# Kernel optimization log

Hardware: AMD Instinct MI355X
Metric: run time of the kernel (lower is better)

## Reference

```python
import jax, jax.numpy as jnp
import numpy as np
from jax import lax

STATE_SIZE = 80
HIDDEN = 512
NC = 1
H = W = 32
STEPS = 64  # steps_range=(64,64)
THRESH = 0.01


def _maxpool3(x):
    # MaxPool2d(3, stride=1, padding=1) on NCHW
    return lax.reduce_window(x, -jnp.inf, lax.max, (1, 1, 3, 3), (1, 1, 1, 1), 'SAME')


def _conv3x3(x, w, b):
    y = lax.conv_general_dilated(x, w, (1, 1), 'SAME',
                                 dimension_numbers=('NCHW', 'OIHW', 'NCHW'))
    return y + b[None, :, None, None]


def _conv1x1(x, w, b):
    # w: (O, I, 1, 1) -> pointwise einsum
    return jnp.einsum('oi,bihw->bohw', w[:, :, 0, 0], x) + b[None, :, None, None]


def setup_inputs() -> dict:
    key = jax.random.key(0)
    ks = jax.random.split(key, 7)
    z = jax.random.normal(ks[0], (8, 100, 1, 1), dtype=jnp.float32)
    W1 = jax.random.normal(ks[1], (HIDDEN, STATE_SIZE, 3, 3), jnp.float32) / np.sqrt(STATE_SIZE * 9)
    b1 = jax.random.normal(ks[2], (HIDDEN,), jnp.float32) * 0.01
    W2 = jax.random.normal(ks[3], (HIDDEN, HIDDEN, 1, 1), jnp.float32) / np.sqrt(HIDDEN)
    b2 = jax.random.normal(ks[4], (HIDDEN,), jnp.float32) * 0.01
    # original code zero-inits the last conv; use small random weights so grads flow
    W3 = jax.random.normal(ks[5], (STATE_SIZE, HIDDEN, 1, 1), jnp.float32) * (0.01 / np.sqrt(HIDDEN))
    b3 = jax.random.normal(ks[6], (STATE_SIZE,), jnp.float32) * 0.001
    return {'z': z, 'W1': W1, 'b1': b1, 'W2': W2, 'b2': b2, 'W3': W3, 'b3': b3}


def _forward(z, W1, b1, W2, b2, W3, b3):
    N = z.shape[0]
    cH, cW = H // 2, W // 2
    state = jnp.zeros((N, STATE_SIZE, H, W), dtype=z.dtype)
    init_hidden = z[:, :STATE_SIZE - 1, 0, 0]  # (N, 79)
    state = state.at[:, 1:, cH, cW].set(init_hidden)
    state = state.at[:, 0, cH, cW].set(1.0)

    keys = jax.random.split(jax.random.key(42), STEPS)

    def ca_step(state, step_key):
        pre_living = _maxpool3(state[:, 0:1]) > THRESH
        perception = _conv3x3(state, W1, b1)
        h = jax.nn.relu(_conv1x1(perception, W2, b2))
        updates = _conv1x1(h, W3, b3)
        # stochastic update with p=1 (rand < 1 is always True, kept for fidelity)
        mask = jax.random.uniform(step_key, (state.shape[0], 1, H, W)) < 1.0
        state = state + mask.astype(state.dtype) * updates
        post_living = _maxpool3(state[:, 0:1]) > THRESH
        living = (post_living & pre_living).astype(state.dtype)
        return state * living, None

    state, _ = lax.scan(ca_step, state, keys)
    return state[:, :NC]  # (N, 1, H, W)


def reference(z, W1, b1, W2, b2, W3, b3):
    return _forward(z, W1, b1, W2, b2, W3, b3)
```

## Files before the change

### kernel.cpp

```cpp
#include <hip/hip_runtime.h>


#define NPIX 8192
#define T_ALIVE 0.01f

typedef _Float16 f16;
typedef __attribute__((ext_vector_type(8)))  _Float16 h8_t;
typedef __attribute__((ext_vector_type(4)))  _Float16 h4_t;
typedef __attribute__((ext_vector_type(16))) float    fx16;

__global__ __launch_bounds__(256) void tr512(
    const float* __restrict__ W2, float* __restrict__ W2T)
{
    __shared__ float t[32][33];
    const int bx = blockIdx.x & 15, by = blockIdx.x >> 4;
    const int x = threadIdx.x & 31, y8 = threadIdx.x >> 5;
#pragma unroll
    for (int r = 0; r < 32; r += 8)
        t[r + y8][x] = W2[(size_t)(by * 32 + r + y8) * 512 + bx * 32 + x];
    __syncthreads();
#pragma unroll
    for (int r = 0; r < 32; r += 8)
        W2T[(size_t)(bx * 32 + r + y8) * 512 + by * 32 + x] = t[x][r + y8];
}

__global__ __launch_bounds__(256) void wc32(
    const float* __restrict__ W2T, const float* __restrict__ W1,
    float* __restrict__ Wc)
{
    __shared__ float As[16][32];
    __shared__ float Bs[16][32];
    const int tid = threadIdx.x;
    const int ty = tid >> 3, tx = tid & 7;
    const int m0 = blockIdx.y * 32, n0 = blockIdx.x * 32;
    float acc[4] = {0.f, 0.f, 0.f, 0.f};

    for (int k0 = 0; k0 < 512; k0 += 16) {
#pragma unroll
        for (int t = 0; t < 2; ++t) {
            const int idx = tid + t * 256;
            const int r = idx >> 5, c = idx & 31;
            As[r][c] = W2T[(size_t)(k0 + r) * 512 + m0 + c];
            const int n = n0 + c;
            Bs[r][c] = (n < 720) ? W1[(size_t)(k0 + r) * 720 + n] : 0.f;
        }
        __syncthreads();
#pragma unroll
        for (int kk = 0; kk < 16; ++kk) {
            const float a = As[kk][ty];
#pragma unroll
            for (int j = 0; j < 4; ++j)
                acc[j] = fmaf(a, Bs[kk][tx * 4 + j], acc[j]);
        }
        __syncthreads();
    }
    const int m = m0 + ty;
#pragma unroll
    for (int j = 0; j < 4; ++j) {
        const int n = n0 + tx * 4 + j;
        if (n < 720) Wc[(size_t)m * 720 + n] = acc[j];
    }
}

__global__ __launch_bounds__(256) void bc_k(
    const float* __restrict__ W2, const float* __restrict__ b1,
    const float* __restrict__ b2, float* __restrict__ bc)
{
    const int m = blockIdx.x * 256 + threadIdx.x;
    if (m >= 512) return;
    float a = b2[m];
    for (int h = 0; h < 512; ++h) a += W2[m * 512 + h] * b1[h];
    bc[m] = a;
}

__global__ __launch_bounds__(256) void swz_wc2(
    const float* __restrict__ Wc, f16* __restrict__ Wcsw2)
{
    const int idx = blockIdx.x * 256 + threadIdx.x;
    if (idx >= 45 * 16 * 64) return;
    const int lane = idx & 63;
    const int t = idx >> 6;
    const int mtg = t & 15, ks = t >> 4;
    const int m = mtg * 32 + (lane & 31);
    const int k0 = ks * 16 + (lane >> 5) * 8;
    h8_t v;
#pragma unroll
    for (int j = 0; j < 8; ++j) {
        const int kp = k0 + j;
        const int tap = kp / 80, ci = kp - tap * 80;
        v[j] = (f16)Wc[(size_t)m * 720 + ci * 9 + tap];
    }
    *(h8_t*)(Wcsw2 + (size_t)idx * 8) = v;
}

__global__ __launch_bounds__(256) void swz_w32(
    const float* __restrict__ W3, f16* __restrict__ W3sw2)
{
    const int idx = blockIdx.x * 256 + threadIdx.x;
    if (idx >= 32 * 3 * 64) return;
    const int lane = idx & 63;
    const int t = idx >> 6;
    const int mt = t % 3, ks2 = t / 3;
    const int m = mt * 32 + (lane & 31);
    const int k0 = ks2 * 16 + (lane >> 5) * 8;
    h8_t v;
#pragma unroll
    for (int j = 0; j < 8; ++j)
        v[j] = (f16)((m < 80) ? W3[(size_t)m * 512 + k0 + j] : 0.f);
    *(h8_t*)(W3sw2 + (size_t)idx * 8) = v;
}

__global__ __launch_bounds__(256) void seed_k(
    const float* __restrict__ z, float* __restrict__ Sf32,
    f16* __restrict__ Smf16)
{
    const int idx = blockIdx.x * 256 + threadIdx.x;
    if (idx >= 640) return;
    const int b = idx / 80, c = idx - b * 80;
    const int n = b * 1024 + 16 * 32 + 16;
    const float v = (c == 0) ? 1.f : z[b * 100 + (c - 1)];
    Sf32[(size_t)c * NPIX + n] = v;
    Smf16[(size_t)n * 80 + c] = (f16)v;
}

__global__ __launch_bounds__(512) void kA(
    const f16* __restrict__ Smf16, const f16* __restrict__ Wcsw2,
    const float* __restrict__ bc, const f16* __restrict__ W3sw2,
    const float* __restrict__ b3,
    const float* __restrict__ Sold, float* __restrict__ U)
{
    __shared__ f16   msT[8160];
    __shared__ f16   Hsw[16384];
    __shared__ float bcL[512];
    __shared__ float b3L[80];

    const int tid = threadIdx.x;
    const int lane = tid & 63, w = tid >> 6;
    const int li = lane & 31, q2 = lane >> 5;
    const int blk = blockIdx.x;
    const int b = blk >> 5, y = blk & 31;
    const int gb = b * 1024;

    if (tid < 512) bcL[tid] = bc[tid];
    if (tid < 80)  b3L[tid] = b3[tid];

    for (int idx = tid; idx < 1020; idx += 512) {
        const int p = idx / 10, cc = idx - p * 10;
        const int r = p / 34, xi = p - r * 34;
        const int gx = xi - 1, yy = y - 1 + r;
        h8_t v;
        if (((unsigned)yy < 32u) & ((unsigned)gx < 32u)) {
            v = *(const h8_t*)(Smf16 + (size_t)(gb + yy * 32 + gx) * 80 + cc * 8);
        } else {
#pragma unroll
            for (int j = 0; j < 8; ++j) v[j] = (f16)0.f;
        }
        *(h8_t*)(msT + (size_t)(cc * 102 + p) * 8) = v;
    }
    __syncthreads();

    int pxh[9];
#pragma unroll
    for (int t = 0; t < 9; ++t)
        pxh[t] = ((t / 3) * 34 + li + (t % 3)) * 8;

    fx16 acc[2];
#pragma unroll
    for (int i = 0; i < 2; ++i)
#pragma unroll
        for (int r = 0; r < 16; ++r) acc[i][r] = 0.f;

    h8_t abuf[8][2];
#pragma unroll
    for (int pk = 0; pk < 8; ++pk)
#pragma unroll
        for (int i = 0; i < 2; ++i)
            abuf[pk][i] = *(const h8_t*)(Wcsw2 +
                (((size_t)pk * 16 + (w * 2 + i)) * 64 + lane) * 8);

#pragma unroll
    for (int ks = 0; ks < 45; ++ks) {
        const int o0 = 2 * ks, o1 = 2 * ks + 1;
        const int a0 = (o0 % 10) * 816 + pxh[o0 / 10];
        const int a1 = (o1 % 10) * 816 + pxh[o1 / 10];
        const h8_t bf = *(const h8_t*)(msT + (q2 ? a1 : a0));
        h8_t av[2];
#pragma unroll
        for (int i = 0; i < 2; ++i) av[i] = abuf[ks & 7][i];
        if (ks + 8 < 45) {
#pragma unroll
            for (int i = 0; i < 2; ++i)
                abuf[ks & 7][i] = *(const h8_t*)(Wcsw2 +
                    (((size_t)(ks + 8) * 16 + (w * 2 + i)) * 64 + lane) * 8);
        }
#pragma unroll
        for (int i = 0; i < 2; ++i)
            acc[i] = __builtin_amdgcn_mfma_f32_32x32x16_f16(
                av[i], bf, acc[i], 0, 0, 0);
    }

#pragma unroll
    for (int i = 0; i < 2; ++i) {
#pragma unroll
        for (int aa = 0; aa < 4; ++aa) {
            const int chl = i * 32 + 8 * aa + 4 * q2;
            const int co = w * 8 + i * 4 + aa;
            h4_t v4;
#pragma unroll
            for (int rb = 0; rb < 4; ++rb)
                v4[rb] = (f16)fmaxf(acc[i][aa * 4 + rb] + bcL[w * 64 + chl + rb], 0.f);
            *(h4_t*)(Hsw + ((size_t)co * 32 + li) * 8 + 4 * q2) = v4;
        }
    }
    __syncthreads();

    if (w < 3) {
        const int mt = w;
        h8_t ar[8];
#pragma unroll
        for (int pk = 0; pk < 8; ++pk)
            ar[pk] = *(const h8_t*)(W3sw2 +
                (((size_t)pk * 3 + mt) * 64 + lane) * 8);

        fx16 acc3;
#pragma unroll
        for (int r = 0; r < 16; ++r) acc3[r] = 0.f;
#pragma unroll
        for (int ks2 = 0; ks2 < 32; ++ks2) {
            const h8_t bf = *(const h8_t*)(Hsw +
                ((size_t)(ks2 * 2 + q2) * 32 + li) * 8);
            const h8_t a = ar[ks2 & 7];
            if (ks2 + 8 < 32)
                ar[ks2 & 7] = *(const h8_t*)(W3sw2 +
                    (((size_t)(ks2 + 8) * 3 + mt) * 64 + lane) * 8);
            acc3 = __builtin_amdgcn_mfma_f32_32x32x16_f16(a, bf, acc3, 0, 0, 0);
        }

        const size_t px = (size_t)(gb + y * 32 + li);
#pragma unroll
        for (int aa = 0; aa < 4; ++aa)
#pragma unroll
            for (int rb = 0; rb < 4; ++rb) {
                const int ch = mt * 32 + rb + 8 * aa + 4 * q2;
                if (ch < 80) {
                    const size_t idx = (size_t)ch * NPIX + px;
                    U[idx] = Sold[idx] + acc3[aa * 4 + rb] + b3L[ch];
                }
            }
    }
}

__global__ __launch_bounds__(256) void kB(
    const float* __restrict__ U, const float* __restrict__ Sold,
    float* __restrict__ Snew, f16* __restrict__ Smf16,
    float* __restrict__ dout, int last)
{
    __shared__ float alphaO3[96];
    __shared__ float alphaN3[96];
    __shared__ float livef[32];

    const int tid = threadIdx.x;
    const int blk = blockIdx.x;
    const int b = blk >> 5, y = blk & 31;
    const int gb = b * 1024;
    const int base = gb + y * 32;

    if (tid < 96) {
        const int r = tid >> 5, x = tid & 31, yy = y - 1 + r;
        if ((unsigned)yy < 32u) {
            alphaO3[tid] = Sold[gb + yy * 32 + x];
            alphaN3[tid] = U[gb + yy * 32 + x];
        } else {
            alphaO3[tid] = -1e30f;
            alphaN3[tid] = -1e30f;
        }
    }
    __syncthreads();

    if (tid < 32) {
        float mN = -1e30f, mO = -1e30f;
#pragma unroll
        for (int r = 0; r < 3; ++r)
#pragma unroll
            for (int dx = -1; dx <= 1; ++dx) {
                const int xx = tid + dx;
                if ((unsigned)xx < 32u) {
                    mN = fmaxf(mN, alphaN3[r * 32 + xx]);
                    mO = fmaxf(mO, alphaO3[r * 32 + xx]);
                }
            }
        livef[tid] = (mN > T_ALIVE && mO > T_ALIVE) ? 1.f : 0.f;
    }
    __syncthreads();

    for (int q = tid; q < 640; q += 256) {
        const int cq = q >> 5, x = q & 31;
        const float lv = livef[x];
        const size_t pxg = (size_t)(base + x);
        h4_t v4;
        float v0 = 0.f;
#pragma unroll
        for (int rb = 0; rb < 4; ++rb) {
            const int ch = cq * 4 + rb;
            const size_t idx = (size_t)ch * NPIX + pxg;
            const float v = U[idx] * lv;
            Snew[idx] = v;
            v4[rb] = (f16)v;
            if (rb == 0) v0 = v;
        }
        *(h4_t*)(Smf16 + pxg * 80 + cq * 4) = v4;
        if (last && cq == 0) dout[pxg] = v0;
    }
}

extern "C" void kernel_launch(void* const* d_in, const int* in_sizes, int n_in,
                              void* d_out, int out_size, void* d_ws, size_t ws_size,
                              hipStream_t stream)
{
    const float* z  = (const float*)d_in[0];
    const float* W1 = (const float*)d_in[1];
    const float* b1 = (const float*)d_in[2];
    const float* W2 = (const float*)d_in[3];
    const float* b2 = (const float*)d_in[4];
    const float* W3 = (const float*)d_in[5];
    const float* b3 = (const float*)d_in[6];

    char* ws = (char*)d_ws;
    float* S0    = (float*)ws;  ws += (size_t)80 * NPIX * 4;
    float* S1    = (float*)ws;  ws += (size_t)80 * NPIX * 4;
    f16*   Sm0   = (f16*)ws;   ws += (size_t)NPIX * 80 * 2;
    f16*   Sm1   = (f16*)ws;   ws += (size_t)NPIX * 80 * 2;
    float* Ubuf  = (float*)ws;  ws += (size_t)80 * NPIX * 4;
    float* bc    = (float*)ws;  ws += 512 * 4;
    float* Wc    = (float*)ws;  ws += (size_t)512 * 720 * 4;
    float* W2T   = (float*)ws;  ws += (size_t)512 * 512 * 4;
    f16*   Wcsw2 = (f16*)ws;   ws += (size_t)45 * 16 * 64 * 8 * 2;
    f16*   W3sw2 = (f16*)ws;   ws += (size_t)32 * 3 * 64 * 8 * 2;

    hipMemsetAsync(S0, 0, (size_t)80 * NPIX * 4, stream);
    hipMemsetAsync(Sm0, 0, (size_t)NPIX * 80 * 2, stream);
    seed_k<<<3, 256, 0, stream>>>(z, S0, Sm0);
    tr512<<<256, 256, 0, stream>>>(W2, W2T);
    wc32<<<dim3(23, 16), 256, 0, stream>>>(W2T, W1, Wc);
    bc_k<<<2, 256, 0, stream>>>(W2, b1, b2, bc);
    swz_wc2<<<180, 256, 0, stream>>>(Wc, Wcsw2);
    swz_w32<<<24, 256, 0, stream>>>(W3, W3sw2);

    float* Scur = S0;  float* Snxt = S1;
    f16*   Mcur = Sm0; f16*   Mnxt = Sm1;
    for (int s = 0; s < 64; ++s) {
        kA<<<256, 512, 0, stream>>>(Mcur, Wcsw2, bc, W3sw2, b3, Scur, Ubuf);
        kB<<<256, 256, 0, stream>>>(Ubuf, Scur, Snxt, Mnxt,
                                    (float*)d_out, (s == 63) ? 1 : 0);
        float* t = Scur; Scur = Snxt; Snxt = t;
        f16*   m = Mcur; Mcur = Mnxt; Mnxt = m;
    }
}
```

Baseline: 1.143 ms.

## Fuse living-mask update into the compute kernel, dropping separate per-step mask kernel

Merges the per-step mask/writeback kernel into the main conv/MLP kernel. Each block now recomputes the living mask for its 3-row halo from the unmasked update buffer and the previous alive channel, and builds the f16 shared-memory tile directly from fp32 global data. A small final kernel applies the last mask. This halves the launches per step and removes the separate f16 state copy and its round trip, at the cost of redundant halo mask work and strided fp32 gathers into shared memory.

```diff
diff --git a/kernel.cpp b/kernel.cpp
--- a/kernel.cpp
+++ b/kernel.cpp
@@ -110,29 +110,33 @@
     *(h8_t*)(W3sw2 + (size_t)idx * 8) = v;
 }
 
-__global__ __launch_bounds__(256) void seed_k(
-    const float* __restrict__ z, float* __restrict__ Sf32,
-    f16* __restrict__ Smf16)
+__global__ __launch_bounds__(256) void seed2(
+    const float* __restrict__ z, float* __restrict__ U0,
+    float* __restrict__ A0)
 {
     const int idx = blockIdx.x * 256 + threadIdx.x;
     if (idx >= 640) return;
     const int b = idx / 80, c = idx - b * 80;
     const int n = b * 1024 + 16 * 32 + 16;
     const float v = (c == 0) ? 1.f : z[b * 100 + (c - 1)];
-    Sf32[(size_t)c * NPIX + n] = v;
-    Smf16[(size_t)n * 80 + c] = (f16)v;
-}
-
-__global__ __launch_bounds__(512) void kA(
-    const f16* __restrict__ Smf16, const f16* __restrict__ Wcsw2,
-    const float* __restrict__ bc, const f16* __restrict__ W3sw2,
-    const float* __restrict__ b3,
-    const float* __restrict__ Sold, float* __restrict__ U)
+    U0[(size_t)c * NPIX + n] = v;
+    if (c == 0) A0[n] = 1.f;
+}
+
+__global__ __launch_bounds__(512) void kS(
+    const f16* __restrict__ Wcsw2, const float* __restrict__ bc,
+    const f16* __restrict__ W3sw2, const float* __restrict__ b3,
+    const float* __restrict__ Uin, const float* __restrict__ Ain,
+    float* __restrict__ Uout, float* __restrict__ Aout)
 {
     __shared__ f16   msT[8160];
     __shared__ f16   Hsw[16384];
     __shared__ float bcL[512];
     __shared__ float b3L[80];
+    __shared__ float SrowL[2560];
+    __shared__ float N5[160];
+    __shared__ float A5[160];
+    __shared__ float live3[96];
 
     const int tid = threadIdx.x;
     const int lane = tid & 63, w = tid >> 6;
@@ -141,35 +145,6 @@
     const int b = blk >> 5, y = blk & 31;
     const int gb = b * 1024;
 
-    if (tid < 512) bcL[tid] = bc[tid];
-    if (tid < 80)  b3L[tid] = b3[tid];
-
-    for (int idx = tid; idx < 1020; idx += 512) {
-        const int p = idx / 10, cc = idx - p * 10;
-        const int r = p / 34, xi = p - r * 34;
-        const int gx = xi - 1, yy = y - 1 + r;
-        h8_t v;
-        if (((unsigned)yy < 32u) & ((unsigned)gx < 32u)) {
-            v = *(const h8_t*)(Smf16 + (size_t)(gb + yy * 32 + gx) * 80 + cc * 8);
-        } else {
-#pragma unroll
-            for (int j = 0; j < 8; ++j) v[j] = (f16)0.f;
-        }
-        *(h8_t*)(msT + (size_t)(cc * 102 + p) * 8) = v;
-    }
-    __syncthreads();
-
-    int pxh[9];
-#pragma unroll
-    for (int t = 0; t < 9; ++t)
-        pxh[t] = ((t / 3) * 34 + li + (t % 3)) * 8;
-
-    fx16 acc[2];
-#pragma unroll
-    for (int i = 0; i < 2; ++i)
-#pragma unroll
-        for (int r = 0; r < 16; ++r) acc[i][r] = 0.f;
-
     h8_t abuf[8][2];
 #pragma unroll
     for (int pk = 0; pk < 8; ++pk)
@@ -177,6 +152,70 @@
         for (int i = 0; i < 2; ++i)
             abuf[pk][i] = *(const h8_t*)(Wcsw2 +
                 (((size_t)pk * 16 + (w * 2 + i)) * 64 + lane) * 8);
+
+    bcL[tid] = bc[tid];
+    if (tid < 80) b3L[tid] = b3[tid];
+
+    if (tid < 160) {
+        const int r = tid >> 5, x = tid & 31, yy = y - 2 + r;
+        const bool ok = ((unsigned)yy < 32u);
+        N5[tid] = ok ? Uin[gb + yy * 32 + x] : -1e30f;
+        A5[tid] = ok ? Ain[gb + yy * 32 + x] : -1e30f;
+    }
+    {
+        h8_t zz;
+#pragma unroll
+        for (int j = 0; j < 8; ++j) zz[j] = (f16)0.f;
+        for (int i = tid; i < 1020; i += 512)
+            *(h8_t*)(msT + (size_t)i * 8) = zz;
+    }
+    __syncthreads();
+
+    if (tid < 96) {
+        const int r = tid >> 5, x = tid & 31;
+        float mN = -1e30f, mA = -1e30f;
+#pragma unroll
+        for (int rr = 0; rr < 3; ++rr)
+#pragma unroll
+            for (int dx = -1; dx <= 1; ++dx) {
+                const int xx = x + dx;
+                if ((unsigned)xx < 32u) {
+                    mN = fmaxf(mN, N5[(r + rr) * 32 + xx]);
+                    mA = fmaxf(mA, A5[(r + rr) * 32 + xx]);
+                }
+            }
+        live3[tid] = (mN > T_ALIVE && mA > T_ALIVE) ? 1.f : 0.f;
+    }
+    __syncthreads();
+
+#pragma unroll
+    for (int it = 0; it < 15; ++it) {
+        const int e = tid + it * 512;
+        const int x = e & 31;
+        const int t2 = e >> 5;
+        const int r = t2 / 80, ch = t2 - r * 80;
+        const int yy = y - 1 + r;
+        float v = 0.f;
+        if ((unsigned)yy < 32u)
+            v = Uin[(size_t)ch * NPIX + gb + yy * 32 + x] * live3[r * 32 + x];
+        msT[(size_t)((ch >> 3) * 102 + r * 34 + x + 1) * 8 + (ch & 7)] = (f16)v;
+        if (r == 1) {
+            SrowL[ch * 32 + x] = v;
+            if (ch == 0) Aout[gb + y * 32 + x] = v;
+        }
+    }
+    __syncthreads();
+
+    int pxh[9];
+#pragma unroll
+    for (int t = 0; t < 9; ++t)
+        pxh[t] = ((t / 3) * 34 + li + (t % 3)) * 8;
+
+    fx16 acc[2];
+#pragma unroll
+    for (int i = 0; i < 2; ++i)
+#pragma unroll
+        for (int r = 0; r < 16; ++r) acc[i][r] = 0.f;
 
 #pragma unroll
     for (int ks = 0; ks < 45; ++ks) {
@@ -243,73 +282,46 @@
             for (int rb = 0; rb < 4; ++rb) {
                 const int ch = mt * 32 + rb + 8 * aa + 4 * q2;
                 if (ch < 80) {
-                    const size_t idx = (size_t)ch * NPIX + px;
-                    U[idx] = Sold[idx] + acc3[aa * 4 + rb] + b3L[ch];
+                    Uout[(size_t)ch * NPIX + px] =
+                        SrowL[ch * 32 + li] + acc3[aa * 4 + rb] + b3L[ch];
                 }
             }
     }
 }
 
-__global__ __launch_bounds__(256) void kB(
-    const float* __restrict__ U, const float* __restrict__ Sold,
-    float* __restrict__ Snew, f16* __restrict__ Smf16,
-    float* __restrict__ dout, int last)
-{
-    __shared__ float alphaO3[96];
-    __shared__ float alphaN3[96];
-    __shared__ float livef[32];
-
+__global__ __launch_bounds__(128) void kF(
+    const float* __restrict__ Uf, const float* __restrict__ Af,
+    float* __restrict__ dout)
+{
+    __shared__ float N3[96];
+    __shared__ float A3[96];
     const int tid = threadIdx.x;
     const int blk = blockIdx.x;
     const int b = blk >> 5, y = blk & 31;
     const int gb = b * 1024;
-    const int base = gb + y * 32;
 
     if (tid < 96) {
         const int r = tid >> 5, x = tid & 31, yy = y - 1 + r;
-        if ((unsigned)yy < 32u) {
-            alphaO3[tid] = Sold[gb + yy * 32 + x];
-            alphaN3[tid] = U[gb + yy * 32 + x];
-        } else {
-            alphaO3[tid] = -1e30f;
-            alphaN3[tid] = -1e30f;
-        }
+        const bool ok = ((unsigned)yy < 32u);
+        N3[tid] = ok ? Uf[gb + yy * 32 + x] : -1e30f;
+        A3[tid] = ok ? Af[gb + yy * 32 + x] : -1e30f;
     }
     __syncthreads();
 
     if (tid < 32) {
-        float mN = -1e30f, mO = -1e30f;
-#pragma unroll
-        for (int r = 0; r < 3; ++r)
+        float mN = -1e30f, mA = -1e30f;
+#pragma unroll
+        for (int rr = 0; rr < 3; ++rr)
 #pragma unroll
             for (int dx = -1; dx <= 1; ++dx) {
                 const int xx = tid + dx;
                 if ((unsigned)xx < 32u) {
-                    mN = fmaxf(mN, alphaN3[r * 32 + xx]);
-                    mO = fmaxf(mO, alphaO3[r * 32 + xx]);
+                    mN = fmaxf(mN, N3[rr * 32 + xx]);
+                    mA = fmaxf(mA, A3[rr * 32 + xx]);
                 }
             }
-        livef[tid] = (mN > T_ALIVE && mO > T_ALIVE) ? 1.f : 0.f;
-    }
-    __syncthreads();
-
-    for (int q = tid; q < 640; q += 256) {
-        const int cq = q >> 5, x = q & 31;
-        const float lv = livef[x];
-        const size_t pxg = (size_t)(base + x);
-        h4_t v4;
-        float v0 = 0.f;
-#pragma unroll
-        for (int rb = 0; rb < 4; ++rb) {
-            const int ch = cq * 4 + rb;
-            const size_t idx = (size_t)ch * NPIX + pxg;
-            const float v = U[idx] * lv;
-            Snew[idx] = v;
-            v4[rb] = (f16)v;
-            if (rb == 0) v0 = v;
-        }
-        *(h4_t*)(Smf16 + pxg * 80 + cq * 4) = v4;
-        if (last && cq == 0) dout[pxg] = v0;
+        const float lv = (mN > T_ALIVE && mA > T_ALIVE) ? 1.f : 0.f;
+        dout[gb + y * 32 + tid] = Uf[gb + y * 32 + tid] * lv;
     }
 }
 
@@ -326,33 +338,31 @@
     const float* b3 = (const float*)d_in[6];
 
     char* ws = (char*)d_ws;
-    float* S0    = (float*)ws;  ws += (size_t)80 * NPIX * 4;
-    float* S1    = (float*)ws;  ws += (size_t)80 * NPIX * 4;
-    f16*   Sm0   = (f16*)ws;   ws += (size_t)NPIX * 80 * 2;
-    f16*   Sm1   = (f16*)ws;   ws += (size_t)NPIX * 80 * 2;
-    float* Ubuf  = (float*)ws;  ws += (size_t)80 * NPIX * 4;
+    float* U0    = (float*)ws;  ws += (size_t)80 * NPIX * 4;
+    float* U1    = (float*)ws;  ws += (size_t)80 * NPIX * 4;
+    float* A0    = (float*)ws;  ws += (size_t)NPIX * 4;
+    float* A1    = (float*)ws;  ws += (size_t)NPIX * 4;
     float* bc    = (float*)ws;  ws += 512 * 4;
     float* Wc    = (float*)ws;  ws += (size_t)512 * 720 * 4;
     float* W2T   = (float*)ws;  ws += (size_t)512 * 512 * 4;
     f16*   Wcsw2 = (f16*)ws;   ws += (size_t)45 * 16 * 64 * 8 * 2;
     f16*   W3sw2 = (f16*)ws;   ws += (size_t)32 * 3 * 64 * 8 * 2;
 
-    hipMemsetAsync(S0, 0, (size_t)80 * NPIX * 4, stream);
-    hipMemsetAsync(Sm0, 0, (size_t)NPIX * 80 * 2, stream);
-    seed_k<<<3, 256, 0, stream>>>(z, S0, Sm0);
+    hipMemsetAsync(U0, 0, (size_t)80 * NPIX * 4, stream);
+    hipMemsetAsync(A0, 0, (size_t)NPIX * 4, stream);
+    seed2<<<3, 256, 0, stream>>>(z, U0, A0);
     tr512<<<256, 256, 0, stream>>>(W2, W2T);
     wc32<<<dim3(23, 16), 256, 0, stream>>>(W2T, W1, Wc);
     bc_k<<<2, 256, 0, stream>>>(W2, b1, b2, bc);
     swz_wc2<<<180, 256, 0, stream>>>(Wc, Wcsw2);
     swz_w32<<<24, 256, 0, stream>>>(W3, W3sw2);
 
-    float* Scur = S0;  float* Snxt = S1;
-    f16*   Mcur = Sm0; f16*   Mnxt = Sm1;
+    float* Uc = U0;  float* Un = U1;
+    float* Ac = A0;  float* An = A1;
     for (int s = 0; s < 64; ++s) {
-        kA<<<256, 512, 0, stream>>>(Mcur, Wcsw2, bc, W3sw2, b3, Scur, Ubuf);
-        kB<<<256, 256, 0, stream>>>(Ubuf, Scur, Snxt, Mnxt,
-                                    (float*)d_out, (s == 63) ? 1 : 0);
-        float* t = Scur; Scur = Snxt; Snxt = t;
-        f16*   m = Mcur; Mcur = Mnxt; Mnxt = m;
-    }
-}
+        kS<<<256, 512, 0, stream>>>(Wcsw2, bc, W3sw2, b3, Uc, Ac, Un, An);
+        float* t = Uc; Uc = Un; Un = t;
+        float* a = Ac; Ac = An; An = a;
+    }
+    kF<<<256, 128, 0, stream>>>(Uc, Ac, (float*)d_out);
+}
```

Result: no change. 1.126 ms (-1.5%).
